# Optimization experiments

Measured on AMD Instinct MI355X. Metric: run time of the kernel, lower is better.

## Reference

```python
import jax, jax.numpy as jnp
import numpy as np
import functools

# Analytic replacement for the per-scalar torch.autograd.grad loop:
#   linear layer z = h @ W^T  -> Jacobian (stacked grads, then .T) = W^T, shape [in, out]
#   ReLU                      -> diag(z > 0), shape [n, n]
#   final Identity            -> eye(outsize)
# Valid for batch=1, matching the flatten() semantics of the original get_jacobian.

def _forward(x, Ws):
    jacobians = []
    h = x
    n_layers = len(Ws)
    for i, W in enumerate(Ws):
        z = h @ W.T                      # [1, out_i]
        jacobians.append(W.T)            # linear Jacobian [in_i, out_i]
        if i < n_layers - 1:
            mask = (z > 0).astype(z.dtype)
            h = z * mask                 # ReLU
            jacobians.append(jnp.diag(mask[0]))  # diagonal ReLU Jacobian
        else:
            h = z                        # nn.Identity
            jacobians.append(jnp.eye(W.shape[0], dtype=z.dtype))
    DJM = functools.reduce(jnp.matmul, jacobians)  # chain_matmul, [insize, outsize]
    return h, DJM, jacobians


def setup_inputs() -> dict:
    key = jax.random.key(0)
    k = jax.random.split(key, 4)
    insize, hsize, outsize = 2048, 4096, 2048
    x = jax.random.normal(k[0], (1, insize), jnp.float32)
    W1 = jax.random.normal(k[1], (hsize, insize), jnp.float32) / np.float32(np.sqrt(insize))
    W2 = jax.random.normal(k[2], (hsize, hsize), jnp.float32) / np.float32(np.sqrt(hsize))
    W3 = jax.random.normal(k[3], (outsize, hsize), jnp.float32) / np.float32(np.sqrt(hsize))
    return {"x": x, "W1": W1, "W2": W2, "W3": W3}


def reference(x, W1, W2, W3):
    out, DJM, jacs = _forward(x, (W1, W2, W3))
    # Matches torch forward: (x, DJM, jacobians); jacobians flattened into tuple.
    return (out, DJM, *jacs)
```

## Files before the change

### kernel.cpp

```cpp
#include <hip/hip_runtime.h>

typedef __bf16 bf16;
typedef __attribute__((ext_vector_type(8))) __bf16 bf16x8;
typedef __attribute__((ext_vector_type(4))) __bf16 bf16x4;
typedef __attribute__((ext_vector_type(4))) float f32x4;

__global__ __launch_bounds__(256) void mv_relu(const float* __restrict__ W,
    const float* __restrict__ v, float* __restrict__ h, float* __restrict__ m,
    float* __restrict__ z, int K) {
  const int row  = (blockIdx.x * blockDim.x + threadIdx.x) >> 6;
  const int lane = threadIdx.x & 63;
  const float* wr = W + (size_t)row * K;
  float s = 0.f;
  for (int c = lane * 4; c < K; c += 256) {
    const float4 w4 = *(const float4*)(wr + c);
    const float4 v4 = *(const float4*)(v + c);
    s += w4.x * v4.x + w4.y * v4.y + w4.z * v4.z + w4.w * v4.w;
  }
  #pragma unroll
  for (int off = 32; off; off >>= 1) s += __shfl_xor(s, off);
  if (lane == 0) {
    if (h) { h[row] = s > 0.f ? s : 0.f; m[row] = s > 0.f ? 1.f : 0.f; }
    if (z) z[row] = s;
  }
}

__global__ __launch_bounds__(256) void transpose_k(const float* __restrict__ in,
    float* __restrict__ outT, bf16* __restrict__ outT_bf,
    const float* __restrict__ scale, int R, int C) {
  __shared__ float tile[32][33];
  const int tr = blockIdx.y * 32, tc = blockIdx.x * 32;
  const int tx = threadIdx.x, ty = threadIdx.y;
  #pragma unroll
  for (int s = 0; s < 4; ++s)
    tile[ty + s * 8][tx] = in[(size_t)(tr + ty + s * 8) * C + (tc + tx)];
  __syncthreads();
  const float sc = scale ? scale[tr + tx] : 1.f;
  #pragma unroll
  for (int s = 0; s < 4; ++s) {
    const int oc = ty + s * 8;
    const float v = tile[tx][oc];
    const size_t o = (size_t)(tc + oc) * R + (tr + tx);
    outT[o] = v;
    if (outT_bf) outT_bf[o] = (bf16)(v * sc);
  }
}

__global__ __launch_bounds__(256) void diag_fill(float* __restrict__ out,
    const float* __restrict__ d, int n) {
  const size_t i = ((size_t)blockIdx.x * blockDim.x + threadIdx.x) * 4;
  const int row = (int)(i >> (31 - __clz(n)));
  const int c0  = (int)(i & (size_t)(n - 1));
  float4 v = make_float4(0.f, 0.f, 0.f, 0.f);
  const int dpos = row - c0;
  if ((unsigned)dpos < 4u) ((float*)&v)[dpos] = d ? d[row] : 1.f;
  *(float4*)(out + i) = v;
}

__global__ __launch_bounds__(256) void scale_cols_bf(const float* __restrict__ in,
    const float* __restrict__ scale, bf16* __restrict__ out, int cmask) {
  const size_t i = ((size_t)blockIdx.x * blockDim.x + threadIdx.x) * 4;
  const float4 v = *(const float4*)(in + i);
  const int c = (int)(i & (size_t)cmask);
  const float4 s4 = *(const float4*)(scale + c);
  bf16x4 o;
  o[0] = (bf16)(v.x * s4.x); o[1] = (bf16)(v.y * s4.y);
  o[2] = (bf16)(v.z * s4.z); o[3] = (bf16)(v.w * s4.w);
  *(bf16x4*)(out + i) = o;
}

__device__ inline void load_lds16(const bf16* g, bf16* lds) {
  __builtin_amdgcn_global_load_lds(
      (const __attribute__((address_space(1))) void*)g,
      (__attribute__((address_space(3))) void*)lds, 16, 0, 0);
}

template <typename CT>
__global__ __launch_bounds__(256) void gemm_nt(const bf16* __restrict__ A,
    const bf16* __restrict__ B, CT* __restrict__ C, int M, int N, int K) {
  constexpr int BM = 128, BN = 128, BK = 32;
  __shared__ __align__(16) bf16 As[BM * BK];
  __shared__ __align__(16) bf16 Bs[BN * BK];
  const int tid = threadIdx.x, lane = tid & 63, wave = tid >> 6;
  const int wm = wave >> 1, wn = wave & 1;
  const int tm = blockIdx.y, tn = blockIdx.x;

  f32x4 acc[4][4] = {};

  const int ldrow = lane >> 2;
  const int ldk   = (lane & 3) * 8;
  const long arow0 = (long)(tm * BM) * K;
  const long brow0 = (long)(tn * BN) * K;

  for (int kt = 0; kt < K; kt += BK) {
    #pragma unroll
    for (int s = 0; s < 2; ++s) {
      const int chunk = wave * 2 + s;
      const int row = chunk * 16 + ldrow;
      load_lds16(A + arow0 + (long)row * K + kt + ldk, As + chunk * 512);
      load_lds16(B + brow0 + (long)row * K + kt + ldk, Bs + chunk * 512);
    }
    __syncthreads();
    bf16x8 af[4], bfr[4];
    const int ko = (lane >> 4) * 8;
    const int fr = lane & 15;
    #pragma unroll
    for (int f = 0; f < 4; ++f) {
      af[f]  = *(const bf16x8*)(As + (wm * 64 + f * 16 + fr) * BK + ko);
      bfr[f] = *(const bf16x8*)(Bs + (wn * 64 + f * 16 + fr) * BK + ko);
    }
    #pragma unroll
    for (int mf = 0; mf < 4; ++mf)
      #pragma unroll
      for (int nf = 0; nf < 4; ++nf)
        acc[mf][nf] = __builtin_amdgcn_mfma_f32_16x16x32_bf16(
            af[mf], bfr[nf], acc[mf][nf], 0, 0, 0);
    __syncthreads();
  }

  const int cr = (lane >> 4) * 4;
  const int cc = lane & 15;
  #pragma unroll
  for (int mf = 0; mf < 4; ++mf) {
    const int r0 = tm * BM + wm * 64 + mf * 16 + cr;
    #pragma unroll
    for (int nf = 0; nf < 4; ++nf) {
      const long c0 = (long)r0 * N + tn * BN + wn * 64 + nf * 16 + cc;
      #pragma unroll
      for (int r = 0; r < 4; ++r)
        C[c0 + (long)r * N] = (CT)acc[mf][nf][r];
    }
  }
}

extern "C" void kernel_launch(void* const* d_in, const int* in_sizes, int n_in,
                              void* d_out, int out_size, void* d_ws, size_t ws_size,
                              hipStream_t stream) {
  const float* x  = (const float*)d_in[0];
  const float* W1 = (const float*)d_in[1];
  const float* W2 = (const float*)d_in[2];
  const float* W3 = (const float*)d_in[3];
  float* out = (float*)d_out;
  constexpr int IN = 2048, HS = 4096, ON = 2048;

  float* z3   = out;
  float* DJM  = z3 + IN;
  float* jac0 = DJM + (size_t)IN * ON;
  float* jac1 = jac0 + (size_t)IN * HS;
  float* jac2 = jac1 + (size_t)HS * HS;
  float* jac3 = jac2 + (size_t)HS * HS;
  float* jac4 = jac3 + (size_t)HS * HS;
  float* jac5 = jac4 + (size_t)HS * ON;

  char* ws = (char*)d_ws;
  float* h1 = (float*)ws;
  float* m1 = h1 + HS;
  float* h2 = m1 + HS;
  float* m2 = h2 + HS;
  size_t off = 1 << 20;
  bf16* W1Ts = (bf16*)(ws + off); off += (size_t)IN * HS * 2;
  bf16* W2T  = (bf16*)(ws + off); off += (size_t)HS * HS * 2;
  bf16* W3s  = (bf16*)(ws + off); off += (size_t)ON * HS * 2;
  bf16* T1   = (bf16*)(ws + off);

  mv_relu<<<HS * 64 / 256, 256, 0, stream>>>(W1, x,  h1, m1, nullptr, IN);
  mv_relu<<<HS * 64 / 256, 256, 0, stream>>>(W2, h1, h2, m2, nullptr, HS);
  mv_relu<<<ON * 64 / 256, 256, 0, stream>>>(W3, h2, nullptr, nullptr, z3, HS);

  dim3 tb(32, 8);
  transpose_k<<<dim3(IN / 32, HS / 32), tb, 0, stream>>>(W1, jac0, W1Ts, m1, HS, IN);
  transpose_k<<<dim3(HS / 32, HS / 32), tb, 0, stream>>>(W2, jac2, W2T, nullptr, HS, HS);
  transpose_k<<<dim3(HS / 32, ON / 32), tb, 0, stream>>>(W3, jac4, nullptr, nullptr, ON, HS);

  scale_cols_bf<<<(ON * HS / 4) / 256, 256, 0, stream>>>(W3, m2, W3s, HS - 1);

  diag_fill<<<((size_t)HS * HS / 4) / 256, 256, 0, stream>>>(jac1, m1, HS);
  diag_fill<<<((size_t)HS * HS / 4) / 256, 256, 0, stream>>>(jac3, m2, HS);
  diag_fill<<<((size_t)ON * ON / 4) / 256, 256, 0, stream>>>(jac5, nullptr, ON);

  gemm_nt<bf16><<<dim3(HS / 128, ON / 128), 256, 0, stream>>>(W3s, W2T, T1, ON, HS, HS);
  gemm_nt<float><<<dim3(ON / 128, IN / 128), 256, 0, stream>>>(W1Ts, T1, DJM, IN, ON, HS);
}
```

Baseline: 730.7 us.

## Split-K both bf16 GEMMs with partial buffers and separate reduction kernels

Both chain GEMMs now split the K dimension across a grid z axis: 2 slices for the first GEMM and 4 for the second. Each slice writes fp32 partials to workspace, and new elementwise kernels sum them, converting to bf16 for the intermediate or writing fp32 to DJM. The first GEMM previously launched 512 blocks and the second only 256, so this raises block counts to fill the many CUs. The cost is extra global traffic for partial writes and reads plus two additional launches.

Measured after the change: 735.0 us. Within noise of the previous version (+0.6%).

```diff
diff --git a/kernel.cpp b/kernel.cpp
--- a/kernel.cpp
+++ b/kernel.cpp
@@ -69,21 +69,48 @@
   *(bf16x4*)(out + i) = o;
 }
 
+__global__ __launch_bounds__(256) void reduce2_bf(const float* __restrict__ P,
+    bf16* __restrict__ out, size_t L) {
+  const size_t i = ((size_t)blockIdx.x * blockDim.x + threadIdx.x) * 4;
+  const float4 a = *(const float4*)(P + i);
+  const float4 b = *(const float4*)(P + L + i);
+  bf16x4 o;
+  o[0] = (bf16)(a.x + b.x); o[1] = (bf16)(a.y + b.y);
+  o[2] = (bf16)(a.z + b.z); o[3] = (bf16)(a.w + b.w);
+  *(bf16x4*)(out + i) = o;
+}
+
+__global__ __launch_bounds__(256) void reduce4_f32(const float* __restrict__ P,
+    float* __restrict__ out, size_t L) {
+  const size_t i = ((size_t)blockIdx.x * blockDim.x + threadIdx.x) * 4;
+  const float4 a = *(const float4*)(P + i);
+  const float4 b = *(const float4*)(P + L + i);
+  const float4 c = *(const float4*)(P + 2 * L + i);
+  const float4 d = *(const float4*)(P + 3 * L + i);
+  float4 o;
+  o.x = (a.x + b.x) + (c.x + d.x);
+  o.y = (a.y + b.y) + (c.y + d.y);
+  o.z = (a.z + b.z) + (c.z + d.z);
+  o.w = (a.w + b.w) + (c.w + d.w);
+  *(float4*)(out + i) = o;
+}
+
 __device__ inline void load_lds16(const bf16* g, bf16* lds) {
   __builtin_amdgcn_global_load_lds(
       (const __attribute__((address_space(1))) void*)g,
       (__attribute__((address_space(3))) void*)lds, 16, 0, 0);
 }
 
-template <typename CT>
-__global__ __launch_bounds__(256) void gemm_nt(const bf16* __restrict__ A,
-    const bf16* __restrict__ B, CT* __restrict__ C, int M, int N, int K) {
+__global__ __launch_bounds__(256) void gemm_nt_sk(const bf16* __restrict__ A,
+    const bf16* __restrict__ B, float* __restrict__ P, int M, int N, int K,
+    int Ks) {
   constexpr int BM = 128, BN = 128, BK = 32;
   __shared__ __align__(16) bf16 As[BM * BK];
   __shared__ __align__(16) bf16 Bs[BN * BK];
   const int tid = threadIdx.x, lane = tid & 63, wave = tid >> 6;
   const int wm = wave >> 1, wn = wave & 1;
   const int tm = blockIdx.y, tn = blockIdx.x;
+  const int kt0 = blockIdx.z * Ks;
 
   f32x4 acc[4][4] = {};
 
@@ -92,7 +119,7 @@
   const long arow0 = (long)(tm * BM) * K;
   const long brow0 = (long)(tn * BN) * K;
 
-  for (int kt = 0; kt < K; kt += BK) {
+  for (int kt = kt0; kt < kt0 + Ks; kt += BK) {
     #pragma unroll
     for (int s = 0; s < 2; ++s) {
       const int chunk = wave * 2 + s;
@@ -118,6 +145,7 @@
     __syncthreads();
   }
 
+  float* Pz = P + (size_t)blockIdx.z * M * N;
   const int cr = (lane >> 4) * 4;
   const int cc = lane & 15;
   #pragma unroll
@@ -128,7 +156,7 @@
       const long c0 = (long)r0 * N + tn * BN + wn * 64 + nf * 16 + cc;
       #pragma unroll
       for (int r = 0; r < 4; ++r)
-        C[c0 + (long)r * N] = (CT)acc[mf][nf][r];
+        Pz[c0 + (long)r * N] = acc[mf][nf][r];
     }
   }
 }
@@ -161,7 +189,8 @@
   bf16* W1Ts = (bf16*)(ws + off); off += (size_t)IN * HS * 2;
   bf16* W2T  = (bf16*)(ws + off); off += (size_t)HS * HS * 2;
   bf16* W3s  = (bf16*)(ws + off); off += (size_t)ON * HS * 2;
-  bf16* T1   = (bf16*)(ws + off);
+  bf16* T1   = (bf16*)(ws + off); off += (size_t)ON * HS * 2;
+  float* P   = (float*)(ws + off);
 
   mv_relu<<<HS * 64 / 256, 256, 0, stream>>>(W1, x,  h1, m1, nullptr, IN);
   mv_relu<<<HS * 64 / 256, 256, 0, stream>>>(W2, h1, h2, m2, nullptr, HS);
@@ -178,6 +207,8 @@
   diag_fill<<<((size_t)HS * HS / 4) / 256, 256, 0, stream>>>(jac3, m2, HS);
   diag_fill<<<((size_t)ON * ON / 4) / 256, 256, 0, stream>>>(jac5, nullptr, ON);
 
-  gemm_nt<bf16><<<dim3(HS / 128, ON / 128), 256, 0, stream>>>(W3s, W2T, T1, ON, HS, HS);
-  gemm_nt<float><<<dim3(ON / 128, IN / 128), 256, 0, stream>>>(W1Ts, T1, DJM, IN, ON, HS);
-}
+  gemm_nt_sk<<<dim3(HS / 128, ON / 128, 2), 256, 0, stream>>>(W3s, W2T, P, ON, HS, HS, HS / 2);
+  reduce2_bf<<<((size_t)ON * HS / 4) / 256, 256, 0, stream>>>(P, T1, (size_t)ON * HS);
+  gemm_nt_sk<<<dim3(ON / 128, IN / 128, 4), 256, 0, stream>>>(W1Ts, T1, P, IN, ON, HS, HS / 4);
+  reduce4_f32<<<((size_t)IN * ON / 4) / 256, 256, 0, stream>>>(P, DJM, (size_t)IN * ON);
+}
```

## Compact GEMMs to active ReLU units via prefix-scan index gathers

Applied to the files above, without the earlier changes.

Adds a single-block scan that counts the active ReLU units in each hidden layer and records their indices. The weight matrices are gathered into compacted bf16 buffers and the GEMMs run with dynamic N and K read from device metadata, so roughly half the work from zero-masked rows and columns is skipped. The transposes now use float4 loads and stores and no longer produce bf16 copies. The cost is three extra gather passes with scattered reads and a serial single-block scan on the critical path.

After: 642.7 us. 1.14x faster.

```diff
diff --git a/kernel.cpp b/kernel.cpp
--- a/kernel.cpp
+++ b/kernel.cpp
@@ -4,6 +4,7 @@
 typedef __attribute__((ext_vector_type(8))) __bf16 bf16x8;
 typedef __attribute__((ext_vector_type(4))) __bf16 bf16x4;
 typedef __attribute__((ext_vector_type(4))) float f32x4;
+
 
 __global__ __launch_bounds__(256) void mv_relu(const float* __restrict__ W,
     const float* __restrict__ v, float* __restrict__ h, float* __restrict__ m,
@@ -25,25 +26,57 @@
   }
 }
 
-__global__ __launch_bounds__(256) void transpose_k(const float* __restrict__ in,
-    float* __restrict__ outT, bf16* __restrict__ outT_bf,
-    const float* __restrict__ scale, int R, int C) {
+__global__ __launch_bounds__(1024) void scan_meta(const float* __restrict__ m1,
+    const float* __restrict__ m2, int* __restrict__ meta,
+    int* __restrict__ inv1, int* __restrict__ inv2) {
+  __shared__ int sd[1024];
+  const int t = threadIdx.x;
+  #pragma unroll
+  for (int pass = 0; pass < 2; ++pass) {
+    const float* m = pass ? m2 : m1;
+    int* inv = pass ? inv2 : inv1;
+    const float4 v = *(const float4*)(m + t * 4);
+    const int f0 = v.x > 0.f, f1 = v.y > 0.f, f2 = v.z > 0.f, f3 = v.w > 0.f;
+    const int ls = f0 + f1 + f2 + f3;
+    sd[t] = ls;
+    __syncthreads();
+    for (int off = 1; off < 1024; off <<= 1) {
+      const int a = sd[t];
+      const int b = (t >= off) ? sd[t - off] : 0;
+      __syncthreads();
+      sd[t] = a + b;
+      __syncthreads();
+    }
+    int p = sd[t] - ls;
+    const int total = sd[1023];
+    if (f0) inv[p++] = t * 4 + 0;
+    if (f1) inv[p++] = t * 4 + 1;
+    if (f2) inv[p++] = t * 4 + 2;
+    if (f3) inv[p++] = t * 4 + 3;
+    if (t == 0) {
+      if (!pass) { const int Sj = (total + 127) & ~127; meta[0] = Sj; meta[3] = Sj; meta[4] = total; }
+      else       { const int Sk = (total + 31) & ~31;   meta[1] = Sk; meta[5] = total; }
+    }
+    __syncthreads();
+  }
+  if (t == 0) meta[2] = 2048;
+}
+
+__global__ __launch_bounds__(256) void transpose_f32(const float* __restrict__ in,
+    float* __restrict__ outT, int R, int C) {
   __shared__ float tile[32][33];
   const int tr = blockIdx.y * 32, tc = blockIdx.x * 32;
-  const int tx = threadIdx.x, ty = threadIdx.y;
-  #pragma unroll
-  for (int s = 0; s < 4; ++s)
-    tile[ty + s * 8][tx] = in[(size_t)(tr + ty + s * 8) * C + (tc + tx)];
+  const int tid = threadIdx.x;
+  const int lr = tid >> 3, lc4 = (tid & 7) * 4;
+  const float4 v = *(const float4*)(in + (size_t)(tr + lr) * C + tc + lc4);
+  tile[lr][lc4] = v.x; tile[lr][lc4 + 1] = v.y;
+  tile[lr][lc4 + 2] = v.z; tile[lr][lc4 + 3] = v.w;
   __syncthreads();
-  const float sc = scale ? scale[tr + tx] : 1.f;
-  #pragma unroll
-  for (int s = 0; s < 4; ++s) {
-    const int oc = ty + s * 8;
-    const float v = tile[tx][oc];
-    const size_t o = (size_t)(tc + oc) * R + (tr + tx);
-    outT[o] = v;
-    if (outT_bf) outT_bf[o] = (bf16)(v * sc);
-  }
+  const int oc = tid & 31, or4 = (tid >> 5) * 4;
+  float4 w;
+  w.x = tile[or4 + 0][oc]; w.y = tile[or4 + 1][oc];
+  w.z = tile[or4 + 2][oc]; w.w = tile[or4 + 3][oc];
+  *(float4*)(outT + (size_t)(tc + oc) * R + tr + or4) = w;
 }
 
 __global__ __launch_bounds__(256) void diag_fill(float* __restrict__ out,
@@ -57,16 +90,50 @@
   *(float4*)(out + i) = v;
 }
 
-__global__ __launch_bounds__(256) void scale_cols_bf(const float* __restrict__ in,
-    const float* __restrict__ scale, bf16* __restrict__ out, int cmask) {
-  const size_t i = ((size_t)blockIdx.x * blockDim.x + threadIdx.x) * 4;
-  const float4 v = *(const float4*)(in + i);
-  const int c = (int)(i & (size_t)cmask);
-  const float4 s4 = *(const float4*)(scale + c);
+__global__ __launch_bounds__(256) void g_W1c(const float* __restrict__ jac0,
+    const int* __restrict__ inv1, const int* __restrict__ meta,
+    bf16* __restrict__ dst) {
+  const int Sj = meta[0], Nc1 = meta[4];
+  const int jc0 = blockIdx.x * 1024 + threadIdx.x * 4;
+  if (jc0 >= Sj) return;
+  const float* row = jac0 + (size_t)blockIdx.y * 4096;
   bf16x4 o;
-  o[0] = (bf16)(v.x * s4.x); o[1] = (bf16)(v.y * s4.y);
-  o[2] = (bf16)(v.z * s4.z); o[3] = (bf16)(v.w * s4.w);
-  *(bf16x4*)(out + i) = o;
+  #pragma unroll
+  for (int e = 0; e < 4; ++e)
+    o[e] = (jc0 + e < Nc1) ? (bf16)row[inv1[jc0 + e]] : (bf16)0.f;
+  *(bf16x4*)(dst + (size_t)blockIdx.y * Sj + jc0) = o;
+}
+
+__global__ __launch_bounds__(256) void g_W2c(const float* __restrict__ jac2,
+    const int* __restrict__ inv1, const int* __restrict__ inv2,
+    const int* __restrict__ meta, bf16* __restrict__ dst) {
+  const int Sj = meta[0], Sk = meta[1], Nc1 = meta[4], Nc2 = meta[5];
+  const int jc = blockIdx.y;
+  if (jc >= Sj) return;
+  const int kc0 = blockIdx.x * 1024 + threadIdx.x * 4;
+  if (kc0 >= Sk) return;
+  bf16x4 o = {};
+  if (jc < Nc1) {
+    const float* row = jac2 + (size_t)inv1[jc] * 4096;
+    #pragma unroll
+    for (int e = 0; e < 4; ++e)
+      o[e] = (kc0 + e < Nc2) ? (bf16)row[inv2[kc0 + e]] : (bf16)0.f;
+  }
+  *(bf16x4*)(dst + (size_t)jc * Sk + kc0) = o;
+}
+
+__global__ __launch_bounds__(256) void g_W3c(const float* __restrict__ W3,
+    const int* __restrict__ inv2, const int* __restrict__ meta,
+    bf16* __restrict__ dst) {
+  const int Sk = meta[1], Nc2 = meta[5];
+  const int kc0 = blockIdx.x * 1024 + threadIdx.x * 4;
+  if (kc0 >= Sk) return;
+  const float* row = W3 + (size_t)blockIdx.y * 4096;
+  bf16x4 o;
+  #pragma unroll
+  for (int e = 0; e < 4; ++e)
+    o[e] = (kc0 + e < Nc2) ? (bf16)row[inv2[kc0 + e]] : (bf16)0.f;
+  *(bf16x4*)(dst + (size_t)blockIdx.y * Sk + kc0) = o;
 }
 
 __device__ inline void load_lds16(const bf16* g, bf16* lds) {
@@ -76,14 +143,17 @@
 }
 
 template <typename CT>
-__global__ __launch_bounds__(256) void gemm_nt(const bf16* __restrict__ A,
-    const bf16* __restrict__ B, CT* __restrict__ C, int M, int N, int K) {
+__global__ __launch_bounds__(256) void gemm_nt_m(const bf16* __restrict__ A,
+    const bf16* __restrict__ B, CT* __restrict__ C,
+    const int* __restrict__ meta, int nIdx, int kIdx) {
+  const int N = meta[nIdx], K = meta[kIdx];
   constexpr int BM = 128, BN = 128, BK = 32;
+  const int tm = blockIdx.y, tn = blockIdx.x;
+  if (tn * BN >= N) return;
   __shared__ __align__(16) bf16 As[BM * BK];
   __shared__ __align__(16) bf16 Bs[BN * BK];
   const int tid = threadIdx.x, lane = tid & 63, wave = tid >> 6;
   const int wm = wave >> 1, wn = wave & 1;
-  const int tm = blockIdx.y, tn = blockIdx.x;
 
   f32x4 acc[4][4] = {};
 
@@ -157,27 +227,33 @@
   float* m1 = h1 + HS;
   float* h2 = m1 + HS;
   float* m2 = h2 + HS;
+  int* meta = (int*)(ws + (64 << 10));
+  int* inv1 = (int*)(ws + (128 << 10));
+  int* inv2 = (int*)(ws + (192 << 10));
   size_t off = 1 << 20;
-  bf16* W1Ts = (bf16*)(ws + off); off += (size_t)IN * HS * 2;
-  bf16* W2T  = (bf16*)(ws + off); off += (size_t)HS * HS * 2;
-  bf16* W3s  = (bf16*)(ws + off); off += (size_t)ON * HS * 2;
-  bf16* T1   = (bf16*)(ws + off);
+  bf16* W1c = (bf16*)(ws + off); off += (size_t)IN * HS * 2;
+  bf16* W2c = (bf16*)(ws + off); off += (size_t)HS * HS * 2;
+  bf16* W3c = (bf16*)(ws + off); off += (size_t)ON * HS * 2;
+  bf16* T1c = (bf16*)(ws + off);
 
   mv_relu<<<HS * 64 / 256, 256, 0, stream>>>(W1, x,  h1, m1, nullptr, IN);
   mv_relu<<<HS * 64 / 256, 256, 0, stream>>>(W2, h1, h2, m2, nullptr, HS);
   mv_relu<<<ON * 64 / 256, 256, 0, stream>>>(W3, h2, nullptr, nullptr, z3, HS);
 
-  dim3 tb(32, 8);
-  transpose_k<<<dim3(IN / 32, HS / 32), tb, 0, stream>>>(W1, jac0, W1Ts, m1, HS, IN);
-  transpose_k<<<dim3(HS / 32, HS / 32), tb, 0, stream>>>(W2, jac2, W2T, nullptr, HS, HS);
-  transpose_k<<<dim3(HS / 32, ON / 32), tb, 0, stream>>>(W3, jac4, nullptr, nullptr, ON, HS);
-
-  scale_cols_bf<<<(ON * HS / 4) / 256, 256, 0, stream>>>(W3, m2, W3s, HS - 1);
+  scan_meta<<<1, 1024, 0, stream>>>(m1, m2, meta, inv1, inv2);
+
+  transpose_f32<<<dim3(IN / 32, HS / 32), 256, 0, stream>>>(W1, jac0, HS, IN);
+  transpose_f32<<<dim3(HS / 32, HS / 32), 256, 0, stream>>>(W2, jac2, HS, HS);
+  transpose_f32<<<dim3(HS / 32, ON / 32), 256, 0, stream>>>(W3, jac4, ON, HS);
 
   diag_fill<<<((size_t)HS * HS / 4) / 256, 256, 0, stream>>>(jac1, m1, HS);
   diag_fill<<<((size_t)HS * HS / 4) / 256, 256, 0, stream>>>(jac3, m2, HS);
   diag_fill<<<((size_t)ON * ON / 4) / 256, 256, 0, stream>>>(jac5, nullptr, ON);
 
-  gemm_nt<bf16><<<dim3(HS / 128, ON / 128), 256, 0, stream>>>(W3s, W2T, T1, ON, HS, HS);
-  gemm_nt<float><<<dim3(ON / 128, IN / 128), 256, 0, stream>>>(W1Ts, T1, DJM, IN, ON, HS);
-}
+  g_W1c<<<dim3(4, IN), 256, 0, stream>>>(jac0, inv1, meta, W1c);
+  g_W2c<<<dim3(4, HS), 256, 0, stream>>>(jac2, inv1, inv2, meta, W2c);
+  g_W3c<<<dim3(4, ON), 256, 0, stream>>>(W3, inv2, meta, W3c);
+
+  gemm_nt_m<bf16><<<dim3(HS / 128, ON / 128), 256, 0, stream>>>(W3c, W2c, T1c, meta, 0, 1);
+  gemm_nt_m<float><<<dim3(ON / 128, IN / 128), 256, 0, stream>>>(W1c, T1c, DJM, meta, 2, 3);
+}
```
